# Kernel tuning notes

Hardware: AMD Instinct MI355X
Metric: run time of the kernel (lower is better)

The kernel has to match this reference:

```python
import jax, jax.numpy as jnp
import numpy as np

NEG = jnp.float32(-1e30)  # log(0) surrogate


def _ctc_loss(logits, labels, label_lengths):
    """CTC loss matching tf.nn.ctc_loss semantics: softmax applied internally,
    blank index = last class, full logit_length = T, mean over batch.

    logits: [B, T, C] float, labels: [B, L] int (padded), label_lengths: [B] int.
    """
    B, T, C = logits.shape
    blank = C - 1
    logp = jax.nn.log_softmax(logits.astype(jnp.float32), axis=-1)  # [B,T,C]
    L = labels.shape[1]
    S = 2 * L + 1  # extended label: blank, l1, blank, l2, ..., blank

    ext = jnp.full((B, S), blank, dtype=jnp.int32).at[:, 1::2].set(labels.astype(jnp.int32))
    # emission log-probs per extended position: [B, T, S]
    emit = jnp.take_along_axis(logp, jnp.broadcast_to(ext[:, None, :], (B, T, S)), axis=2)

    # skip transition s-2 -> s allowed iff ext[s] is a label differing from ext[s-2]
    prev2 = jnp.pad(ext[:, :-2], ((0, 0), (2, 0)), constant_values=-1)
    allow2 = (ext != blank) & (ext != prev2)  # [B,S]

    ll = label_lengths.astype(jnp.int32)
    valid = jnp.arange(S)[None, :] < (2 * ll[:, None] + 1)  # [B,S]

    # t = 0: only s=0 (blank) and s=1 (first label) reachable
    alpha0 = jnp.full((B, S), NEG)
    alpha0 = alpha0.at[:, 0].set(0.0)
    alpha0 = alpha0.at[:, 1].set(jnp.where(ll > 0, 0.0, NEG))
    alpha0 = jnp.where(valid, alpha0 + emit[:, 0, :], NEG)

    def step(alpha, emit_t):
        s1 = jnp.pad(alpha[:, :-1], ((0, 0), (1, 0)), constant_values=NEG)
        s2 = jnp.pad(alpha[:, :-2], ((0, 0), (2, 0)), constant_values=NEG)
        s2 = jnp.where(allow2, s2, NEG)
        a = jax.scipy.special.logsumexp(jnp.stack([alpha, s1, s2]), axis=0) + emit_t
        a = jnp.where(valid, a, NEG)
        return a, None

    alpha, _ = jax.lax.scan(step, alpha0, jnp.swapaxes(emit, 0, 1)[1:])  # scan over T-1 steps

    # terminate at final blank (s=2*ll) or final label (s=2*ll-1)
    a_end1 = jnp.take_along_axis(alpha, (2 * ll)[:, None], axis=1)[:, 0]
    a_end2 = jnp.take_along_axis(alpha, jnp.maximum(2 * ll - 1, 0)[:, None], axis=1)[:, 0]
    a_end2 = jnp.where(ll > 0, a_end2, NEG)
    loss = -jnp.logaddexp(a_end1, a_end2)  # [B]
    return jnp.mean(loss)


def setup_inputs() -> dict:
    key = jax.random.key(0)
    k1, k2, k3 = jax.random.split(key, 3)
    B, T, L, C = 32, 1024, 128, 801  # C = num_classes + 1 (blank = 800)
    logits = jax.random.normal(k1, (B, T, C), dtype=jnp.float32)
    labels = jax.random.randint(k2, (B, L), 0, 800, dtype=jnp.int32)
    label_lengths = jax.random.randint(k3, (B,), 64, L + 1, dtype=jnp.int32)
    return {"logits": logits, "labels": labels, "label_lengths": label_lengths}


def reference(logits, labels, label_lengths):
    return _ctc_loss(logits, labels, label_lengths)
```

## Files before the change

kernel.cpp:

```cpp
#include <hip/hip_runtime.h>
#include <math.h>

#define B_ 32
#define T_ 1024
#define C_ 801
#define L_ 128
#define S_ 257
#define BLANK 800
#define NEGV -1e30f

#define CH 64
#define NCH (T_ / CH)
#define NW 8
#define LN2F 0.69314718055994531f

typedef const unsigned short __attribute__((address_space(1))) u16_g;
typedef unsigned short __attribute__((address_space(3))) u16_l;

template <int CTRL>
__device__ __forceinline__ float dppf(float v) {
    return __uint_as_float((unsigned)__builtin_amdgcn_update_dpp(
        0, (int)__float_as_uint(v), CTRL, 0xf, 0xf, true));
}
__device__ __forceinline__ float shift_up1(float v) { return dppf<0x138>(v); }

__device__ __forceinline__ float wave_red_max63(float v) {
    v = fmaxf(v, dppf<0xB1>(v));
    v = fmaxf(v, dppf<0x4E>(v));
    v = fmaxf(v, dppf<0x141>(v));
    v = fmaxf(v, dppf<0x140>(v));
    v = fmaxf(v, dppf<0x142>(v));
    v = fmaxf(v, dppf<0x143>(v));
    return v;
}
__device__ __forceinline__ float wave_red_sum63(float v) {
    v += dppf<0xB1>(v);
    v += dppf<0x4E>(v);
    v += dppf<0x141>(v);
    v += dppf<0x140>(v);
    v += dppf<0x142>(v);
    v += dppf<0x143>(v);
    return v;
}
__device__ __forceinline__ float bcast63(float v) {
    return __uint_as_float((unsigned)__builtin_amdgcn_readlane((int)__float_as_uint(v), 63));
}
__device__ __forceinline__ float wave_max_nn(float v) { return bcast63(wave_red_max63(v)); }

__device__ __forceinline__ float bf16_to_f32(unsigned short u) {
    return __uint_as_float((unsigned)u << 16);
}
__device__ __forceinline__ float bf16lo(unsigned u) { return __uint_as_float(u << 16); }
__device__ __forceinline__ float bf16hi(unsigned u) { return __uint_as_float(u & 0xFFFF0000u); }
__device__ __forceinline__ unsigned short f32_to_bf16_rne(float f) {
    unsigned u = __float_as_uint(f);
    u += 0x7FFF + ((u >> 16) & 1);
    return (unsigned short)(u >> 16);
}

__global__ __launch_bounds__(256) void stage_kernel(const float* __restrict__ logits,
                                                    const int* __restrict__ labels,
                                                    const int* __restrict__ lens,
                                                    unsigned short* __restrict__ ea,
                                                    float* __restrict__ eq) {
    const int tid = threadIdx.x, lane = tid & 63, wv = tid >> 6;
    const int b = blockIdx.y;
    const int t0 = blockIdx.x * 4;
    const float* __restrict__ base = logits + ((size_t)b * T_ + t0) * C_;
    __shared__ float xs[4 * C_];

    const float4* src = (const float4*)base;
    #pragma unroll
    for (int k = 0; k < 4; ++k) {
        int idx = tid + 256 * k;
        if (idx < 801) ((float4*)xs)[idx] = src[idx];
    }
    __syncthreads();

    const float* xr = xs + wv * C_;
    float v[13];
    float m = NEGV;
    #pragma unroll
    for (int k = 0; k < 12; ++k) { v[k] = xr[lane + 64 * k]; m = fmaxf(m, v[k]); }
    v[12] = (lane < 33) ? xr[768 + lane] : NEGV;
    m = fmaxf(m, v[12]);
    m = bcast63(wave_red_max63(m));

    float s = 0.f;
    #pragma unroll
    for (int k = 0; k < 13; ++k) s += __expf(v[k] - m);
    s = bcast63(wave_red_sum63(s));
    const float lse = m + __logf(s);

    const int ll = lens[b];
    const int t = t0 + wv;
    const int row = b * T_ + t;
    const int smax = 2 * ll + 1;
    const float ebl = __expf(xr[BLANK] - lse) * 1024.0f;
    const int cls1 = labels[b * L_ + 2 * lane];
    const int cls3 = labels[b * L_ + 2 * lane + 1];
    const int s0 = 4 * lane;
    float e0 = (s0     < smax) ? ebl : 0.f;
    float e1 = (s0 + 1 < smax) ? __expf(xr[cls1] - lse) * 1024.0f : 0.f;
    float e2 = (s0 + 2 < smax) ? ebl : 0.f;
    float e3 = (s0 + 3 < smax) ? __expf(xr[cls3] - lse) * 1024.0f : 0.f;

    ushort4 o;
    o.x = f32_to_bf16_rne(e0);
    o.y = f32_to_bf16_rne(e1);
    o.z = f32_to_bf16_rne(e2);
    o.w = f32_to_bf16_rne(e3);
    *(ushort4*)(ea + ((size_t)(row >> 1)) * 512 + 8 * lane + (row & 1) * 4) = o;

    if (lane == 0) eq[row] = (ll == 128) ? ebl : 0.f;
}


__device__ __forceinline__ void stage_chunk_split(const unsigned short* gbase, int c,
                                                  unsigned short* lbase, int lane, int wid) {
    #pragma unroll
    for (int k = 0; k < 32 / NW; ++k) {
        int i = wid + k * NW;
        const unsigned short* gp = gbase + ((size_t)(c * CH + 2 * i)) * 256 + 8 * lane;
        unsigned short* lp = lbase + i * 512;
        __builtin_amdgcn_global_load_lds((u16_g*)gp, (u16_l*)lp, 16, 0, 0);
    }
}

__device__ __forceinline__ void step5(float ex, float ey, float ez, float ew, float eqt,
                                      float m21, float m23,
                                      float& p0, float& p1, float& p2, float& p3, float& q) {
    float shp3 = shift_up1(p3);
    float n0 = (p0 + shp3) * ex;
    float n1 = fmaf(m21, shp3, p1 + p0) * ey;
    float n2 = (p2 + p1) * ez;
    float n3 = fmaf(m23, p1, p3 + p2) * ew;
    q = (q + p3) * eqt;
    p0 = n0; p1 = n1; p2 = n2; p3 = n3;
}

#define RLANE(x, j) __uint_as_float((unsigned)__builtin_amdgcn_readlane((int)__float_as_uint(x), (j)))

template <int FIRST>
__device__ __forceinline__ void compute_chunk(const unsigned short* bufp, float eqc, int lane,
                                              float m21, float m23,
                                              float& p0, float& p1, float& p2, float& p3,
                                              float& q, int& E) {
    #pragma unroll
    for (int jp = 0; jp < CH / 2; ++jp) {
        uint4 w = *(const uint4*)(bufp + jp * 512 + 8 * lane);
        if (!(FIRST && jp == 0)) {
            step5(bf16lo(w.x), bf16hi(w.x), bf16lo(w.y), bf16hi(w.y),
                  RLANE(eqc, 2 * jp), m21, m23, p0, p1, p2, p3, q);
        }
        step5(bf16lo(w.z), bf16hi(w.z), bf16lo(w.w), bf16hi(w.w),
              RLANE(eqc, 2 * jp + 1), m21, m23, p0, p1, p2, p3, q);
        if ((jp & 3) == 3) {
            float mx = fmaxf(fmaxf(p0, p1), fmaxf(p2, fmaxf(p3, q)));
            mx = wave_max_nn(mx);
            int e2_ = (int)((__float_as_uint(mx) >> 23) & 0xFF) - 126;
            float sc_ = __uint_as_float((unsigned)(127 - e2_) << 23);
            p0 *= sc_; p1 *= sc_; p2 *= sc_; p3 *= sc_; q *= sc_;
            E += e2_;
        }
    }
}

__global__ __launch_bounds__(NW * 64) void ctc_lds_kernel(const unsigned short* __restrict__ ea,
                                                          const float* __restrict__ eqg,
                                                          const int* __restrict__ labels,
                                                          const int* __restrict__ lens,
                                                          float* __restrict__ loss) {
    __shared__ unsigned short buf[2][CH * 256];
    const int b = blockIdx.x;
    const int tid = threadIdx.x;
    const int lane = tid & 63;
    const int wid = tid >> 6;
    const int ll = lens[b];
    const unsigned short* gbase = ea + (size_t)b * T_ * 256;
    const float* qbase = eqg + b * T_;

    float m21 = 0.f, m23 = 0.f;
    if (wid == 0) {
        int s1 = 4 * lane + 1;
        if (s1 >= 3) {
            int li = s1 >> 1;
            m21 = (labels[b * L_ + li] != labels[b * L_ + li - 1]) ? 1.f : 0.f;
        }
        int li3 = (4 * lane + 3) >> 1;
        m23 = (labels[b * L_ + li3] != labels[b * L_ + li3 - 1]) ? 1.f : 0.f;
    }

    stage_chunk_split(gbase, 0, buf[0], lane, wid);
    float eqC = 0.f, eqN = 0.f;
    if (wid == 0) eqC = qbase[lane];
    __syncthreads();

    float p0 = 0.f, p1 = 0.f, p2 = 0.f, p3 = 0.f, q = 0.f;
    if (wid == 0) {
        ushort4 r0 = *(const ushort4*)(&buf[0][8 * lane]);
        p0 = (lane == 0) ? bf16_to_f32(r0.x) : 0.f;
        p1 = (lane == 0) ? bf16_to_f32(r0.y) : 0.f;
    }
    int E = 0;

    #pragma unroll 1
    for (int c = 0; c < NCH; ++c) {
        if (c + 1 < NCH) {
            stage_chunk_split(gbase, c + 1, buf[(c + 1) & 1], lane, wid);
            if (wid == 0) eqN = qbase[(c + 1) * CH + lane];
        }
        if (wid == 0) {
            if (c == 0) compute_chunk<1>(buf[0],     eqC, lane, m21, m23, p0, p1, p2, p3, q, E);
            else        compute_chunk<0>(buf[c & 1], eqC, lane, m21, m23, p0, p1, p2, p3, q, E);
            eqC = eqN;
        }
        __syncthreads();
    }

    float* pf = (float*)(&buf[0][0]);
    if (wid == 0) {
        *(float4*)(pf + 4 * lane) = make_float4(p0, p1, p2, p3);
        if (lane == 63) pf[256] = q;
    }
    __syncthreads();
    if (tid == 0) {
        float a1 = pf[2 * ll];
        float a2 = (ll > 0) ? pf[2 * ll - 1] : 0.f;
        loss[b] = -(__logf(a1 + a2) + ((float)E - 10240.0f) * LN2F);
    }
}

__global__ void mean_kernel(const float* __restrict__ loss, float* __restrict__ out) {
    if (threadIdx.x == 0) {
        float s = 0.f;
        for (int i = 0; i < B_; ++i) s += loss[i];
        out[0] = s / (float)B_;
    }
}


__global__ __launch_bounds__(256) void lse_kernel(const float* __restrict__ logits,
                                                  float* __restrict__ lse) {
    const int row = blockIdx.x;
    const float* __restrict__ x = logits + (size_t)row * C_;
    const int tid = threadIdx.x, lane = tid & 63, wid = tid >> 6;
    float v0 = x[tid], v1 = x[tid + 256], v2 = x[tid + 512];
    bool h3 = (tid + 768) < C_;
    float v3 = h3 ? x[tid + 768] : NEGV;
    float m = fmaxf(fmaxf(v0, v1), fmaxf(v2, v3));
    #pragma unroll
    for (int off = 32; off > 0; off >>= 1) m = fmaxf(m, __shfl_down(m, off));
    __shared__ float wred[4]; __shared__ float bm;
    if (lane == 0) wred[wid] = m;
    __syncthreads();
    if (tid == 0) bm = fmaxf(fmaxf(wred[0], wred[1]), fmaxf(wred[2], wred[3]));
    __syncthreads();
    m = bm;
    float s = __expf(v0 - m) + __expf(v1 - m) + __expf(v2 - m);
    if (h3) s += __expf(v3 - m);
    #pragma unroll
    for (int off = 32; off > 0; off >>= 1) s += __shfl_down(s, off);
    __syncthreads();
    if (lane == 0) wred[wid] = s;
    __syncthreads();
    if (tid == 0) lse[row] = m + __logf(wred[0] + wred[1] + wred[2] + wred[3]);
}

__global__ __launch_bounds__(320) void ctc_alpha_kernel(const float* __restrict__ logits,
                                                        const int* __restrict__ labels,
                                                        const int* __restrict__ lens,
                                                        const float* __restrict__ lse,
                                                        float* __restrict__ loss) {
    const int b = blockIdx.x;
    const int s = threadIdx.x;
    const int ll = lens[b];
    __shared__ float albuf[2][S_ + 2];
    if (s < 2) { albuf[0][s] = NEGV; albuf[1][s] = NEGV; }
    int cls = BLANK; bool allow2 = false;
    if (s < S_ && (s & 1)) {
        cls = labels[b * L_ + (s >> 1)];
        allow2 = (s >= 3) && (cls != labels[b * L_ + (s >> 1) - 1]);
    }
    const bool valid = (s < 2 * ll + 1);
    const float* __restrict__ xb = logits + (size_t)b * T_ * C_;
    const float* __restrict__ lseb = lse + b * T_;
    if (s < S_) {
        float e0 = xb[cls] - lseb[0];
        float a = (s == 0 || (s == 1 && ll > 0)) ? e0 : NEGV;
        if (!valid) a = NEGV;
        albuf[0][2 + s] = a;
    }
    __syncthreads();
    float e_next = xb[(size_t)C_ + cls];
    float lse_next = lseb[1];
    int cur = 0;
    for (int t = 1; t < T_; ++t) {
        const float e = e_next, lse_t = lse_next;
        if (t + 1 < T_) { e_next = xb[(size_t)(t + 1) * C_ + cls]; lse_next = lseb[t + 1]; }
        if (s < S_) {
            float a0 = albuf[cur][2 + s];
            float a1 = albuf[cur][1 + s];
            float a2 = allow2 ? albuf[cur][s] : NEGV;
            float m = fmaxf(fmaxf(a0, a1), a2);
            float r = m + __logf(__expf(a0 - m) + __expf(a1 - m) + __expf(a2 - m)) + (e - lse_t);
            if (!valid) r = NEGV;
            albuf[cur ^ 1][2 + s] = r;
        }
        __syncthreads();
        cur ^= 1;
    }
    if (s == 0) {
        float a1 = albuf[cur][2 + 2 * ll];
        float a2 = (ll > 0) ? albuf[cur][2 + 2 * ll - 1] : NEGV;
        float m = fmaxf(a1, a2);
        loss[b] = -(m + __logf(__expf(a1 - m) + __expf(a2 - m)));
    }
}


extern "C" void kernel_launch(void* const* d_in, const int* in_sizes, int n_in,
                              void* d_out, int out_size, void* d_ws, size_t ws_size,
                              hipStream_t stream) {
    const float* logits = (const float*)d_in[0];
    const int*   labels = (const int*)d_in[1];
    const int*   lens   = (const int*)d_in[2];
    float* out = (float*)d_out;

    const size_t ea_elems = (size_t)B_ * T_ * 256;
    const size_t eq_elems = (size_t)B_ * T_;
    const size_t need = ea_elems * 2 + (eq_elems + B_) * 4;

    if (ws_size >= need) {
        unsigned short* ea = (unsigned short*)d_ws;
        float* eq   = (float*)(ea + ea_elems);
        float* loss = eq + eq_elems;
        dim3 grid(T_ / 4, B_);
        stage_kernel<<<grid, 256, 0, stream>>>(logits, labels, lens, ea, eq);
        ctc_lds_kernel<<<B_, NW * 64, 0, stream>>>(ea, eq, labels, lens, loss);
        mean_kernel<<<1, 64, 0, stream>>>(loss, out);
    } else {
        float* lse  = (float*)d_ws;
        float* loss = lse + (size_t)B_ * T_;
        lse_kernel<<<B_ * T_, 256, 0, stream>>>(logits, lse);
        ctc_alpha_kernel<<<B_, 320, 0, stream>>>(logits, labels, lens, lse, loss);
        mean_kernel<<<1, 64, 0, stream>>>(loss, out);
    }
}
```

Measured before the change: 78.67 us.

## Store only label emissions in workspace and broadcast blank emission per timestep

The staging kernel now writes only the two label emissions per lane (packed bf16) plus one blank emission per row, instead of four bf16 values per lane that repeated the blank. The recurrence rebuilds the blank terms from the broadcast scalar using per-lane validity masks, so intermediate traffic is halved. The chunk size doubles to 128 timesteps, and renormalisation now runs every 8 steps. The cost is more multiplies per step in the serial loop and a change in numeric scaling behaviour.

```diff
diff --git a/kernel.cpp b/kernel.cpp
--- a/kernel.cpp
+++ b/kernel.cpp
@@ -9,13 +9,13 @@
 #define BLANK 800
 #define NEGV -1e30f
 
-#define CH 64
+#define CH 128
 #define NCH (T_ / CH)
 #define NW 8
 #define LN2F 0.69314718055994531f
 
-typedef const unsigned short __attribute__((address_space(1))) u16_g;
-typedef unsigned short __attribute__((address_space(3))) u16_l;
+typedef const unsigned __attribute__((address_space(1))) u32_g;
+typedef unsigned __attribute__((address_space(3))) u32_l;
 
 template <int CTRL>
 __device__ __forceinline__ float dppf(float v) {
@@ -47,9 +47,6 @@
 }
 __device__ __forceinline__ float wave_max_nn(float v) { return bcast63(wave_red_max63(v)); }
 
-__device__ __forceinline__ float bf16_to_f32(unsigned short u) {
-    return __uint_as_float((unsigned)u << 16);
-}
 __device__ __forceinline__ float bf16lo(unsigned u) { return __uint_as_float(u << 16); }
 __device__ __forceinline__ float bf16hi(unsigned u) { return __uint_as_float(u & 0xFFFF0000u); }
 __device__ __forceinline__ unsigned short f32_to_bf16_rne(float f) {
@@ -58,11 +55,13 @@
     return (unsigned short)(u >> 16);
 }
 
+#define RLANE(x, j) __uint_as_float((unsigned)__builtin_amdgcn_readlane((int)__float_as_uint(x), (j)))
+
 __global__ __launch_bounds__(256) void stage_kernel(const float* __restrict__ logits,
                                                     const int* __restrict__ labels,
                                                     const int* __restrict__ lens,
-                                                    unsigned short* __restrict__ ea,
-                                                    float* __restrict__ eq) {
+                                                    unsigned* __restrict__ ea32,
+                                                    float* __restrict__ ebq) {
     const int tid = threadIdx.x, lane = tid & 63, wv = tid >> 6;
     const int b = blockIdx.y;
     const int t0 = blockIdx.x * 4;
@@ -93,94 +92,83 @@
     const float lse = m + __logf(s);
 
     const int ll = lens[b];
-    const int t = t0 + wv;
-    const int row = b * T_ + t;
-    const int smax = 2 * ll + 1;
+    const int row = b * T_ + (t0 + wv);
     const float ebl = __expf(xr[BLANK] - lse) * 1024.0f;
     const int cls1 = labels[b * L_ + 2 * lane];
     const int cls3 = labels[b * L_ + 2 * lane + 1];
-    const int s0 = 4 * lane;
-    float e0 = (s0     < smax) ? ebl : 0.f;
-    float e1 = (s0 + 1 < smax) ? __expf(xr[cls1] - lse) * 1024.0f : 0.f;
-    float e2 = (s0 + 2 < smax) ? ebl : 0.f;
-    float e3 = (s0 + 3 < smax) ? __expf(xr[cls3] - lse) * 1024.0f : 0.f;
-
-    ushort4 o;
-    o.x = f32_to_bf16_rne(e0);
-    o.y = f32_to_bf16_rne(e1);
-    o.z = f32_to_bf16_rne(e2);
-    o.w = f32_to_bf16_rne(e3);
-    *(ushort4*)(ea + ((size_t)(row >> 1)) * 512 + 8 * lane + (row & 1) * 4) = o;
-
-    if (lane == 0) eq[row] = (ll == 128) ? ebl : 0.f;
-}
-
-
-__device__ __forceinline__ void stage_chunk_split(const unsigned short* gbase, int c,
-                                                  unsigned short* lbase, int lane, int wid) {
-    #pragma unroll
-    for (int k = 0; k < 32 / NW; ++k) {
-        int i = wid + k * NW;
-        const unsigned short* gp = gbase + ((size_t)(c * CH + 2 * i)) * 256 + 8 * lane;
-        unsigned short* lp = lbase + i * 512;
-        __builtin_amdgcn_global_load_lds((u16_g*)gp, (u16_l*)lp, 16, 0, 0);
-    }
-}
-
-__device__ __forceinline__ void step5(float ex, float ey, float ez, float ew, float eqt,
-                                      float m21, float m23,
-                                      float& p0, float& p1, float& p2, float& p3, float& q) {
-    float shp3 = shift_up1(p3);
-    float n0 = (p0 + shp3) * ex;
-    float n1 = fmaf(m21, shp3, p1 + p0) * ey;
-    float n2 = (p2 + p1) * ez;
-    float n3 = fmaf(m23, p1, p3 + p2) * ew;
-    q = (q + p3) * eqt;
-    p0 = n0; p1 = n1; p2 = n2; p3 = n3;
-}
-
-#define RLANE(x, j) __uint_as_float((unsigned)__builtin_amdgcn_readlane((int)__float_as_uint(x), (j)))
+    float e1 = (2 * lane     < ll) ? __expf(xr[cls1] - lse) * 1024.0f : 0.f;
+    float e3 = (2 * lane + 1 < ll) ? __expf(xr[cls3] - lse) * 1024.0f : 0.f;
+
+    unsigned pack = ((unsigned)f32_to_bf16_rne(e3) << 16) | (unsigned)f32_to_bf16_rne(e1);
+    ea32[(size_t)row * 64 + lane] = pack;
+    if (lane == 0) ebq[row] = ebl;
+}
+
+
+__device__ __forceinline__ void stage_chunk_split(const unsigned* gbase, int c,
+                                                  unsigned* lbase, int lane, int wid) {
+    #pragma unroll
+    for (int k = 0; k < CH / NW; ++k) {
+        int r = wid + k * NW;
+        const unsigned* gp = gbase + ((size_t)(c * CH + r)) * 64 + lane;
+        unsigned* lp = lbase + r * 64;
+        __builtin_amdgcn_global_load_lds((u32_g*)gp, (u32_l*)lp, 4, 0, 0);
+    }
+}
 
 template <int FIRST>
-__device__ __forceinline__ void compute_chunk(const unsigned short* bufp, float eqc, int lane,
-                                              float m21, float m23,
+__device__ __forceinline__ void compute_chunk(const unsigned* bufp, float ebv0, float ebv1,
+                                              int lane, float m21, float m23,
+                                              float mask0, float mask2, float kq,
                                               float& p0, float& p1, float& p2, float& p3,
                                               float& q, int& E) {
     #pragma unroll
-    for (int jp = 0; jp < CH / 2; ++jp) {
-        uint4 w = *(const uint4*)(bufp + jp * 512 + 8 * lane);
-        if (!(FIRST && jp == 0)) {
-            step5(bf16lo(w.x), bf16hi(w.x), bf16lo(w.y), bf16hi(w.y),
-                  RLANE(eqc, 2 * jp), m21, m23, p0, p1, p2, p3, q);
-        }
-        step5(bf16lo(w.z), bf16hi(w.z), bf16lo(w.w), bf16hi(w.w),
-              RLANE(eqc, 2 * jp + 1), m21, m23, p0, p1, p2, p3, q);
-        if ((jp & 3) == 3) {
-            float mx = fmaxf(fmaxf(p0, p1), fmaxf(p2, fmaxf(p3, q)));
-            mx = wave_max_nn(mx);
-            int e2_ = (int)((__float_as_uint(mx) >> 23) & 0xFF) - 126;
-            float sc_ = __uint_as_float((unsigned)(127 - e2_) << 23);
-            p0 *= sc_; p1 *= sc_; p2 *= sc_; p3 *= sc_; q *= sc_;
-            E += e2_;
-        }
-    }
-}
-
-__global__ __launch_bounds__(NW * 64) void ctc_lds_kernel(const unsigned short* __restrict__ ea,
-                                                          const float* __restrict__ eqg,
+    for (int g = 0; g < CH / 8; ++g) {
+        unsigned u[8];
+        #pragma unroll
+        for (int k = 0; k < 8; ++k) u[k] = bufp[(g * 8 + k) * 64 + lane];
+        #pragma unroll
+        for (int k = 0; k < 8; ++k) {
+            if (FIRST && g == 0 && k == 0) continue;
+            const int j = g * 8 + k;
+            float ebt = (j < 64) ? RLANE(ebv0, j) : RLANE(ebv1, j - 64);
+            float el0 = bf16lo(u[k]);
+            float el1 = bf16hi(u[k]);
+            float ebm0 = ebt * mask0;
+            float ebm2 = ebt * mask2;
+            float eqm  = ebt * kq;
+            float shp3 = shift_up1(p3);
+            float n0 = (p0 + shp3) * ebm0;
+            float n1 = fmaf(m21, shp3, p1 + p0) * el0;
+            float n2 = (p2 + p1) * ebm2;
+            float n3 = fmaf(m23, p1, p3 + p2) * el1;
+            q = (q + p3) * eqm;
+            p0 = n0; p1 = n1; p2 = n2; p3 = n3;
+        }
+        float mx = fmaxf(fmaxf(p0, p1), fmaxf(p2, fmaxf(p3, q)));
+        mx = wave_max_nn(mx);
+        int e2_ = (int)((__float_as_uint(mx) >> 23) & 0xFF) - 126;
+        float sc_ = __uint_as_float((unsigned)(127 - e2_) << 23);
+        p0 *= sc_; p1 *= sc_; p2 *= sc_; p3 *= sc_; q *= sc_;
+        E += e2_;
+    }
+}
+
+__global__ __launch_bounds__(NW * 64) void ctc_lds_kernel(const unsigned* __restrict__ ea32,
+                                                          const float* __restrict__ ebq,
                                                           const int* __restrict__ labels,
                                                           const int* __restrict__ lens,
                                                           float* __restrict__ loss) {
-    __shared__ unsigned short buf[2][CH * 256];
+    __shared__ unsigned buf[2][CH * 64];
     const int b = blockIdx.x;
     const int tid = threadIdx.x;
     const int lane = tid & 63;
     const int wid = tid >> 6;
     const int ll = lens[b];
-    const unsigned short* gbase = ea + (size_t)b * T_ * 256;
-    const float* qbase = eqg + b * T_;
-
-    float m21 = 0.f, m23 = 0.f;
+    const unsigned* gbase = ea32 + (size_t)b * T_ * 64;
+    const float* qb = ebq + b * T_;
+
+    float m21 = 0.f, m23 = 0.f, mask0 = 0.f, mask2 = 0.f, kq = 0.f;
     if (wid == 0) {
         int s1 = 4 * lane + 1;
         if (s1 >= 3) {
@@ -189,18 +177,23 @@
         }
         int li3 = (4 * lane + 3) >> 1;
         m23 = (labels[b * L_ + li3] != labels[b * L_ + li3 - 1]) ? 1.f : 0.f;
+        const int smax = 2 * ll + 1;
+        mask0 = (4 * lane     < smax) ? 1.f : 0.f;
+        mask2 = (4 * lane + 2 < smax) ? 1.f : 0.f;
+        kq    = (ll == 128) ? 1.f : 0.f;
     }
 
     stage_chunk_split(gbase, 0, buf[0], lane, wid);
-    float eqC = 0.f, eqN = 0.f;
-    if (wid == 0) eqC = qbase[lane];
+    float ebv0 = 0.f, ebv1 = 0.f, ebn0 = 0.f, ebn1 = 0.f;
+    if (wid == 0) { ebv0 = qb[lane]; ebv1 = qb[64 + lane]; }
     __syncthreads();
 
     float p0 = 0.f, p1 = 0.f, p2 = 0.f, p3 = 0.f, q = 0.f;
     if (wid == 0) {
-        ushort4 r0 = *(const ushort4*)(&buf[0][8 * lane]);
-        p0 = (lane == 0) ? bf16_to_f32(r0.x) : 0.f;
-        p1 = (lane == 0) ? bf16_to_f32(r0.y) : 0.f;
+        float eb0 = RLANE(ebv0, 0);
+        unsigned w0 = buf[0][lane];
+        p0 = (lane == 0) ? eb0 : 0.f;
+        p1 = (lane == 0) ? bf16lo(w0) : 0.f;
     }
     int E = 0;
 
@@ -208,12 +201,14 @@
     for (int c = 0; c < NCH; ++c) {
         if (c + 1 < NCH) {
             stage_chunk_split(gbase, c + 1, buf[(c + 1) & 1], lane, wid);
-            if (wid == 0) eqN = qbase[(c + 1) * CH + lane];
+            if (wid == 0) { ebn0 = qb[(c + 1) * CH + lane]; ebn1 = qb[(c + 1) * CH + 64 + lane]; }
         }
         if (wid == 0) {
-            if (c == 0) compute_chunk<1>(buf[0],     eqC, lane, m21, m23, p0, p1, p2, p3, q, E);
-            else        compute_chunk<0>(buf[c & 1], eqC, lane, m21, m23, p0, p1, p2, p3, q, E);
-            eqC = eqN;
+            if (c == 0) compute_chunk<1>(buf[0],     ebv0, ebv1, lane, m21, m23,
+                                         mask0, mask2, kq, p0, p1, p2, p3, q, E);
+            else        compute_chunk<0>(buf[c & 1], ebv0, ebv1, lane, m21, m23,
+                                         mask0, mask2, kq, p0, p1, p2, p3, q, E);
+            ebv0 = ebn0; ebv1 = ebn1;
         }
         __syncthreads();
     }
@@ -327,17 +322,17 @@
     const int*   lens   = (const int*)d_in[2];
     float* out = (float*)d_out;
 
-    const size_t ea_elems = (size_t)B_ * T_ * 256;
-    const size_t eq_elems = (size_t)B_ * T_;
-    const size_t need = ea_elems * 2 + (eq_elems + B_) * 4;
+    const size_t ea_elems = (size_t)B_ * T_ * 64;
+    const size_t eb_elems = (size_t)B_ * T_;
+    const size_t need = (ea_elems + eb_elems + B_) * 4;
 
     if (ws_size >= need) {
-        unsigned short* ea = (unsigned short*)d_ws;
-        float* eq   = (float*)(ea + ea_elems);
-        float* loss = eq + eq_elems;
+        unsigned* ea32 = (unsigned*)d_ws;
+        float* ebq  = (float*)(ea32 + ea_elems);
+        float* loss = ebq + eb_elems;
         dim3 grid(T_ / 4, B_);
-        stage_kernel<<<grid, 256, 0, stream>>>(logits, labels, lens, ea, eq);
-        ctc_lds_kernel<<<B_, NW * 64, 0, stream>>>(ea, eq, labels, lens, loss);
+        stage_kernel<<<grid, 256, 0, stream>>>(logits, labels, lens, ea32, ebq);
+        ctc_lds_kernel<<<B_, NW * 64, 0, stream>>>(ea32, ebq, labels, lens, loss);
         mean_kernel<<<1, 64, 0, stream>>>(loss, out);
     } else {
         float* lse  = (float*)d_ws;
```

After: 73.93 us. 1.06x faster.
